# Optimization experiments

Measured on AMD Instinct MI355X. Metric: run time of the kernel, lower is better.

Reference implementation:

```python
import jax, jax.numpy as jnp
import numpy as np
import math

D_MODEL = 512
D_K = 64
B, S = 8, 2048
NEG_INF = -1.0e9


def setup_inputs() -> dict:
    key = jax.random.key(0)
    ks = jax.random.split(key, 10)
    inp = {
        "query_source": jax.random.normal(ks[0], (B, S, D_MODEL), dtype=jnp.float32),
        "key_source": jax.random.normal(ks[1], (B, S, D_MODEL), dtype=jnp.float32),
        "value_source": jax.random.normal(ks[2], (B, S, D_MODEL), dtype=jnp.float32),
        # causal mask: 1 means "masked" (future positions), matching masked_fill(mask == 1, -1e9)
        "mask": jnp.triu(jnp.ones((S, S), dtype=jnp.int32), k=1),
        # Linear weights stored as [in, out] so x @ W + b matches torch Linear
        "Wq": jax.random.normal(ks[3], (D_MODEL, D_K), dtype=jnp.float32) / math.sqrt(D_MODEL),
        "bq": jax.random.normal(ks[4], (D_K,), dtype=jnp.float32) * 0.01,
        "Wk": jax.random.normal(ks[5], (D_MODEL, D_K), dtype=jnp.float32) / math.sqrt(D_MODEL),
        "bk": jax.random.normal(ks[6], (D_K,), dtype=jnp.float32) * 0.01,
        "Wv": jax.random.normal(ks[7], (D_MODEL, D_K), dtype=jnp.float32) / math.sqrt(D_MODEL),
        "bv": jax.random.normal(ks[8], (D_K,), dtype=jnp.float32) * 0.01,
    }
    return inp


def reference(query_source, key_source, value_source, mask, Wq, bq, Wk, bk, Wv, bv):
    d_k = Wq.shape[-1]
    Q = query_source @ Wq + bq          # [B, S, d_k]
    K = key_source @ Wk + bk            # [B, S, d_k]
    V = value_source @ Wv + bv          # [B, S, d_k]
    scores = jnp.einsum("bqd,bkd->bqk", Q, K) / jnp.sqrt(jnp.float32(d_k))  # [B, S, S]
    scores = jnp.where(mask == 1, jnp.float32(NEG_INF), scores)
    attn = jax.nn.softmax(scores, axis=-1)
    return jnp.einsum("bqk,bkd->bqd", attn, V)  # [B, S, d_k]
```

## Files before the change

kernel.cpp:

```cpp
#include <hip/hip_runtime.h>

#define BATCH 8
#define SEQ 2048
#define DMODEL 512
#define DK 64

typedef __attribute__((ext_vector_type(8))) short short8;
typedef __attribute__((ext_vector_type(4))) float f32x4;

__device__ __forceinline__ unsigned f2bfbits(float f) {
  unsigned u = __builtin_bit_cast(unsigned, f);
  return (u + 0x7FFFu + ((u >> 16) & 1u)) >> 16;
}

__device__ __forceinline__ void glds16(const void* g, void* l) {
  __builtin_amdgcn_global_load_lds(
      (const __attribute__((address_space(1))) unsigned int*)g,
      (__attribute__((address_space(3))) unsigned int*)l, 16, 0, 0);
}

#define MFMA_BF16(a, b, c) __builtin_amdgcn_mfma_f32_16x16x32_bf16((a), (b), (c), 0, 0, 0)

__global__ __launch_bounds__(256) void wtrans_kernel(
    const float* __restrict__ Wq, const float* __restrict__ Wk,
    const float* __restrict__ Wv, unsigned short* __restrict__ Wt)
{
  const int p = blockIdx.y;
  const float* W = (p == 0) ? Wq : (p == 1) ? Wk : Wv;
  const int t = threadIdx.x;
  const int c = t & 63;
  const int k0 = blockIdx.x * 64 + (t >> 6) * 16;
  unsigned short* dst = Wt + (p * 64 + c) * 512;
  #pragma unroll
  for (int i = 0; i < 16; ++i) {
    int k = k0 + i;
    dst[k] = (unsigned short)f2bfbits(W[k * 64 + c]);
  }
}

__global__ __launch_bounds__(256) void proj_kernel(
    const float* __restrict__ Xq, const float* __restrict__ Xk, const float* __restrict__ Xv,
    const unsigned short* __restrict__ Wt,
    const float* __restrict__ bq, const float* __restrict__ bk, const float* __restrict__ bv,
    unsigned short* __restrict__ oq, unsigned short* __restrict__ ok,
    unsigned short* __restrict__ ov)
{
  __shared__ __attribute__((aligned(16))) short xs[2][64 * 128];
  __shared__ __attribute__((aligned(16))) short wt[2][64 * 128];

  const int p = blockIdx.y;
  const float* X    = (p == 0) ? Xq : (p == 1) ? Xk : Xv;
  const float* bias = (p == 0) ? bq : (p == 1) ? bk : bv;
  unsigned short* out = (p == 0) ? oq : (p == 1) ? ok : ov;
  const float scale = (p == 0) ? 0.125f : 1.0f;
  const unsigned short* Wtp = Wt + p * 64 * 512;

  const int tid = threadIdx.x;
  const long row0 = (long)blockIdx.x * 64;
  const int w = tid >> 6, lane = tid & 63, m = lane & 15, quad = lane >> 4;
  const int xm = m & 7;

  f32x4 acc[4];
  #pragma unroll
  for (int c = 0; c < 4; ++c) acc[c] = (f32x4){0.f, 0.f, 0.f, 0.f};

  auto stage = [&](int buf, int k0) {
    #pragma unroll
    for (int t = 0; t < 4; ++t) {
      int row = w * 16 + t * 4 + (lane >> 4);
      int lc = (lane & 15) ^ (row & 7);
      glds16(Wtp + row * 512 + k0 + lc * 8, &wt[buf][(w * 16 + t * 4) * 128]);
    }
    #pragma unroll
    for (int i = 0; i < 4; ++i) {
      int row = (tid >> 4) + 16 * i;
      int lc = tid & 15;
      const float* xp = X + (row0 + row) * DMODEL + k0 + lc * 8;
      float4 v0 = *(const float4*)xp;
      float4 v1 = *(const float4*)(xp + 4);
      uint4 pk;
      pk.x = f2bfbits(v0.x) | (f2bfbits(v0.y) << 16);
      pk.y = f2bfbits(v0.z) | (f2bfbits(v0.w) << 16);
      pk.z = f2bfbits(v1.x) | (f2bfbits(v1.y) << 16);
      pk.w = f2bfbits(v1.z) | (f2bfbits(v1.w) << 16);
      int pc = lc ^ (row & 7);
      *(uint4*)&xs[buf][row * 128 + pc * 8] = pk;
    }
  };

  stage(0, 0);

  #pragma unroll
  for (int h = 0; h < 4; ++h) {
    __syncthreads();
    if (h < 3) stage((h + 1) & 1, (h + 1) * 128);

    const short* xb = &xs[h & 1][0];
    const short* wb = &wt[h & 1][0];
    #pragma unroll
    for (int s = 0; s < 4; ++s) {
      const int ch0 = ((s * 4 + quad) ^ xm) * 8;
      short8 aF = *(const short8*)&xb[(w * 16 + m) * 128 + ch0];
      #pragma unroll
      for (int c = 0; c < 4; ++c) {
        short8 bF = *(const short8*)&wb[(c * 16 + m) * 128 + ch0];
        acc[c] = MFMA_BF16(aF, bF, acc[c]);
      }
    }
  }

  float bbv[4];
  #pragma unroll
  for (int c = 0; c < 4; ++c) bbv[c] = bias[c * 16 + m];

  if (p < 2) {
    #pragma unroll
    for (int c = 0; c < 4; ++c) {
      #pragma unroll
      for (int r = 0; r < 4; ++r) {
        long row = row0 + w * 16 + quad * 4 + r;
        float v = (acc[c][r] + bbv[c]) * scale;
        out[row * DK + c * 16 + m] = (unsigned short)f2bfbits(v);
      }
    }
  } else {
    long b = row0 >> 11;
    int sbase = (int)(row0 & 2047) + w * 16 + quad * 4;
    #pragma unroll
    for (int c = 0; c < 4; ++c) {
      unsigned lo = f2bfbits(acc[c][0] + bbv[c]) | (f2bfbits(acc[c][1] + bbv[c]) << 16);
      unsigned hi = f2bfbits(acc[c][2] + bbv[c]) | (f2bfbits(acc[c][3] + bbv[c]) << 16);
      *(uint2*)(out + ((long)(b * 64 + c * 16 + m)) * SEQ + sbase) = make_uint2(lo, hi);
    }
  }
}

__global__ __launch_bounds__(256) void attn_kernel(
    const unsigned short* __restrict__ Qb,
    const unsigned short* __restrict__ Kb,
    const unsigned short* __restrict__ Vtg,
    unsigned short* __restrict__ Opart,
    float* __restrict__ lpart,
    float* __restrict__ out)
{
  __shared__ __attribute__((aligned(16))) short ks[2][64 * 64];
  __shared__ __attribute__((aligned(16))) short vt[2][64 * 64];
  __shared__ __attribute__((aligned(16))) short ps[4][16 * 72];

  const int tid = threadIdx.x;
  const int bi = blockIdx.x & 7;
  const int j = blockIdx.x >> 3;

  int qt = 0, c = 0;
  {
    int jj = j;
    for (qt = 0; qt < 32; ++qt) {
      int cnt = (qt >> 2) + 1;
      if (jj < cnt) { c = jj; break; }
      jj -= cnt;
    }
  }
  const int q0 = qt << 6;
  const int kt0 = c << 2;
  const int ntc = min(4, qt + 1 - (c << 2));

  const int w = tid >> 6, lane = tid & 63, m = lane & 15, quad = lane >> 4;
  const int xm = m & 7;

  const int qrow = q0 + w * 16 + m;
  const unsigned short* qp = Qb + ((long)(bi * SEQ + qrow)) * DK + quad * 8;
  const short8 qA0 = *(const short8*)qp;
  const short8 qA1 = *(const short8*)(qp + 32);

  f32x4 o[4];
  #pragma unroll
  for (int d = 0; d < 4; ++d) o[d] = (f32x4){0.f, 0.f, 0.f, 0.f};
  float psum[4] = {0.f, 0.f, 0.f, 0.f};

  const int srow = lane >> 3;
  const int slc  = (lane & 7) ^ srow;

  auto stage = [&](int buf, int ktg) {
    const int k0 = ktg << 6;
    #pragma unroll
    for (int t = 0; t < 2; ++t) {
      const int row = w * 16 + t * 8 + srow;
      glds16(Kb + ((long)(bi * SEQ + k0 + row)) * DK + slc * 8,
             &ks[buf][(w * 16 + t * 8) * 64]);
      glds16(Vtg + ((long)(bi * DK + row)) * SEQ + k0 + slc * 8,
             &vt[buf][(w * 16 + t * 8) * 64]);
    }
  };

  stage(0, kt0);

  for (int i = 0; i < ntc; ++i) {
    __syncthreads();
    if (i + 1 < ntc) stage((i + 1) & 1, kt0 + i + 1);

    const int ktg = kt0 + i;
    const short* ksb = &ks[i & 1][0];
    const short* vtb = &vt[i & 1][0];

    f32x4 sc[4];
    #pragma unroll
    for (int cc = 0; cc < 4; ++cc) {
      const short* kr = ksb + (cc * 16 + m) * 64;
      f32x4 a = {0.f, 0.f, 0.f, 0.f};
      a = MFMA_BF16(qA0, *(const short8*)(kr + ((quad ^ xm) * 8)), a);
      a = MFMA_BF16(qA1, *(const short8*)(kr + (((4 + quad) ^ xm) * 8)), a);
      sc[cc] = a;
    }

    if (ktg == qt) {
      const int rb = q0 + w * 16 + quad * 4;
      const int k0g = ktg << 6;
      #pragma unroll
      for (int cc = 0; cc < 4; ++cc) {
        const int col = k0g + cc * 16 + m;
        #pragma unroll
        for (int r = 0; r < 4; ++r)
          if (col > rb + r) sc[cc][r] = -1e9f;
      }
    }

    #pragma unroll
    for (int cc = 0; cc < 4; ++cc) {
      #pragma unroll
      for (int r = 0; r < 4; ++r)
        sc[cc][r] = __expf(sc[cc][r]);
    }
    #pragma unroll
    for (int r = 0; r < 4; ++r)
      psum[r] += (sc[0][r] + sc[1][r]) + (sc[2][r] + sc[3][r]);

    short* pw = &ps[w][0];
    #pragma unroll
    for (int cc = 0; cc < 4; ++cc) {
      #pragma unroll
      for (int r = 0; r < 4; ++r)
        pw[(quad * 4 + r) * 72 + cc * 16 + m] = (short)f2bfbits(sc[cc][r]);
    }
    asm volatile("s_waitcnt lgkmcnt(0)" ::: "memory");

    const short8 pA0 = *(const short8*)(pw + m * 72 + quad * 8);
    const short8 pA1 = *(const short8*)(pw + m * 72 + quad * 8 + 32);

    #pragma unroll
    for (int d = 0; d < 4; ++d) {
      const short* vr = vtb + (d * 16 + m) * 64;
      o[d] = MFMA_BF16(pA0, *(const short8*)(vr + ((quad ^ xm) * 8)), o[d]);
      o[d] = MFMA_BF16(pA1, *(const short8*)(vr + (((4 + quad) ^ xm) * 8)), o[d]);
    }
  }

  #pragma unroll
  for (int off = 1; off < 16; off <<= 1) {
    #pragma unroll
    for (int r = 0; r < 4; ++r)
      psum[r] += __shfl_xor(psum[r], off);
  }

  const int rb = w * 16 + quad * 4;
  if (qt < 4) {
    #pragma unroll
    for (int r = 0; r < 4; ++r) {
      const float inv = 1.0f / psum[r];
      float* op = out + ((long)(bi * SEQ + q0 + rb + r)) * DK + m;
      op[0]  = o[0][r] * inv;
      op[16] = o[1][r] * inv;
      op[32] = o[2][r] * inv;
      op[48] = o[3][r] * inv;
    }
  } else {
    const int pi = bi * 144 + j;
    unsigned short* opp = Opart + (long)pi * 4096;
    #pragma unroll
    for (int r = 0; r < 4; ++r) {
      unsigned short* op = opp + (rb + r) * 64 + m;
      op[0]  = (unsigned short)f2bfbits(o[0][r]);
      op[16] = (unsigned short)f2bfbits(o[1][r]);
      op[32] = (unsigned short)f2bfbits(o[2][r]);
      op[48] = (unsigned short)f2bfbits(o[3][r]);
    }
    if (m == 0) {
      #pragma unroll
      for (int r = 0; r < 4; ++r)
        lpart[pi * 64 + rb + r] = psum[r];
    }
  }
}

__global__ __launch_bounds__(256) void combine_kernel(
    const unsigned short* __restrict__ Opart, const float* __restrict__ lpart,
    float* __restrict__ out)
{
  const int bi = blockIdx.x & 7;
  const int qt = (blockIdx.x >> 3) + 4;
  const int g = qt >> 2, r = qt & 3;
  const int base = bi * 144 + (g + 1) * (2 * g + r);
  const int cnt = g + 1;

  __shared__ float linv[64];
  const int tid = threadIdx.x;
  if (tid < 64) {
    float s = 0.f;
    for (int i = 0; i < cnt; ++i) s += lpart[(base + i) * 64 + tid];
    linv[tid] = 1.0f / s;
  }
  __syncthreads();

  const int row = tid >> 2;
  const int col0 = (tid & 3) << 4;
  float a[16];
  #pragma unroll
  for (int k = 0; k < 16; ++k) a[k] = 0.f;

  for (int i = 0; i < cnt; ++i) {
    const uint4* op = (const uint4*)(Opart + (long)(base + i) * 4096 + row * 64 + col0);
    uint4 t0 = op[0], t1 = op[1];
    const unsigned uu[8] = {t0.x, t0.y, t0.z, t0.w, t1.x, t1.y, t1.z, t1.w};
    #pragma unroll
    for (int k = 0; k < 8; ++k) {
      a[2 * k]     += __builtin_bit_cast(float, uu[k] << 16);
      a[2 * k + 1] += __builtin_bit_cast(float, uu[k] & 0xFFFF0000u);
    }
  }

  const float inv = linv[row];
  float4* dst = (float4*)(out + ((long)(bi * SEQ + (qt << 6) + row)) * DK + col0);
  #pragma unroll
  for (int k = 0; k < 4; ++k)
    dst[k] = make_float4(a[4*k] * inv, a[4*k+1] * inv, a[4*k+2] * inv, a[4*k+3] * inv);
}

extern "C" void kernel_launch(void* const* d_in, const int* in_sizes, int n_in,
                              void* d_out, int out_size, void* d_ws, size_t ws_size,
                              hipStream_t stream) {
  const float* qs   = (const float*)d_in[0];
  const float* ksrc = (const float*)d_in[1];
  const float* vsrc = (const float*)d_in[2];
  const float* Wq = (const float*)d_in[4];
  const float* bq = (const float*)d_in[5];
  const float* Wk = (const float*)d_in[6];
  const float* bk = (const float*)d_in[7];
  const float* Wv = (const float*)d_in[8];
  const float* bv = (const float*)d_in[9];

  unsigned short* Qb  = (unsigned short*)d_ws;
  unsigned short* Kb  = Qb + (long)BATCH * SEQ * DK;
  unsigned short* Vtg = Kb + (long)BATCH * SEQ * DK;
  unsigned short* Opart = Vtg + (long)BATCH * SEQ * DK;
  float* lpart = (float*)(Opart + (long)1152 * 64 * 64);
  unsigned short* Wtg = (unsigned short*)d_out;
  float* outp = (float*)d_out;

  wtrans_kernel<<<dim3(8, 3), dim3(256), 0, stream>>>(Wq, Wk, Wv, Wtg);
  proj_kernel<<<dim3(256, 3), dim3(256), 0, stream>>>(
      qs, ksrc, vsrc, Wtg, bq, bk, bv, Qb, Kb, Vtg);
  attn_kernel<<<dim3(1152), dim3(256), 0, stream>>>(Qb, Kb, Vtg, Opart, lpart, outp);
  combine_kernel<<<dim3(224), dim3(256), 0, stream>>>(Opart, lpart, outp);
}
```

Before: 177.7 us.

## Load projection operands directly from global into MFMA registers, drop LDS staging

The projection kernel no longer stages X and transposed W tiles through double-buffered shared memory with barriers. Each lane loads its A fragment straight from global fp32 memory, converts it to bf16 in registers, and reads its B fragments directly from the bf16 weight buffer. This removes LDS traffic, swizzling and __syncthreads overhead. In exchange each wave now re-reads the weight fragments from global/L2, and the loads are less coalesced and not overlapped by explicit prefetch.

Result: slower. 187.3 us (+5.4%).

```diff
diff --git a/kernel.cpp b/kernel.cpp
--- a/kernel.cpp
+++ b/kernel.cpp
@@ -45,9 +45,6 @@
     unsigned short* __restrict__ oq, unsigned short* __restrict__ ok,
     unsigned short* __restrict__ ov)
 {
-  __shared__ __attribute__((aligned(16))) short xs[2][64 * 128];
-  __shared__ __attribute__((aligned(16))) short wt[2][64 * 128];
-
   const int p = blockIdx.y;
   const float* X    = (p == 0) ? Xq : (p == 1) ? Xk : Xv;
   const float* bias = (p == 0) ? bq : (p == 1) ? bk : bv;
@@ -58,54 +55,28 @@
   const int tid = threadIdx.x;
   const long row0 = (long)blockIdx.x * 64;
   const int w = tid >> 6, lane = tid & 63, m = lane & 15, quad = lane >> 4;
-  const int xm = m & 7;
+
+  const float* xp = X + (row0 + w * 16 + m) * DMODEL + quad * 8;
+  const unsigned short* wp = Wtp + m * 512 + quad * 8;
 
   f32x4 acc[4];
   #pragma unroll
   for (int c = 0; c < 4; ++c) acc[c] = (f32x4){0.f, 0.f, 0.f, 0.f};
 
-  auto stage = [&](int buf, int k0) {
-    #pragma unroll
-    for (int t = 0; t < 4; ++t) {
-      int row = w * 16 + t * 4 + (lane >> 4);
-      int lc = (lane & 15) ^ (row & 7);
-      glds16(Wtp + row * 512 + k0 + lc * 8, &wt[buf][(w * 16 + t * 4) * 128]);
-    }
-    #pragma unroll
-    for (int i = 0; i < 4; ++i) {
-      int row = (tid >> 4) + 16 * i;
-      int lc = tid & 15;
-      const float* xp = X + (row0 + row) * DMODEL + k0 + lc * 8;
-      float4 v0 = *(const float4*)xp;
-      float4 v1 = *(const float4*)(xp + 4);
-      uint4 pk;
-      pk.x = f2bfbits(v0.x) | (f2bfbits(v0.y) << 16);
-      pk.y = f2bfbits(v0.z) | (f2bfbits(v0.w) << 16);
-      pk.z = f2bfbits(v1.x) | (f2bfbits(v1.y) << 16);
-      pk.w = f2bfbits(v1.z) | (f2bfbits(v1.w) << 16);
-      int pc = lc ^ (row & 7);
-      *(uint4*)&xs[buf][row * 128 + pc * 8] = pk;
-    }
-  };
-
-  stage(0, 0);
-
-  #pragma unroll
-  for (int h = 0; h < 4; ++h) {
-    __syncthreads();
-    if (h < 3) stage((h + 1) & 1, (h + 1) * 128);
-
-    const short* xb = &xs[h & 1][0];
-    const short* wb = &wt[h & 1][0];
-    #pragma unroll
-    for (int s = 0; s < 4; ++s) {
-      const int ch0 = ((s * 4 + quad) ^ xm) * 8;
-      short8 aF = *(const short8*)&xb[(w * 16 + m) * 128 + ch0];
-      #pragma unroll
-      for (int c = 0; c < 4; ++c) {
-        short8 bF = *(const short8*)&wb[(c * 16 + m) * 128 + ch0];
-        acc[c] = MFMA_BF16(aF, bF, acc[c]);
-      }
+  #pragma unroll
+  for (int s = 0; s < 16; ++s) {
+    float4 v0 = *(const float4*)(xp + s * 32);
+    float4 v1 = *(const float4*)(xp + s * 32 + 4);
+    uint4 pk;
+    pk.x = f2bfbits(v0.x) | (f2bfbits(v0.y) << 16);
+    pk.y = f2bfbits(v0.z) | (f2bfbits(v0.w) << 16);
+    pk.z = f2bfbits(v1.x) | (f2bfbits(v1.y) << 16);
+    pk.w = f2bfbits(v1.z) | (f2bfbits(v1.w) << 16);
+    const short8 aF = __builtin_bit_cast(short8, pk);
+    #pragma unroll
+    for (int c = 0; c < 4; ++c) {
+      const short8 bF = *(const short8*)(wp + (c * 16) * 512 + s * 32);
+      acc[c] = MFMA_BF16(aF, bF, acc[c]);
     }
   }
 
```
